# Optimization experiments

Hardware: AMD Instinct MI355X
Metric: run time of the kernel (lower is better)

The kernel has to match this reference:

```python
import jax, jax.numpy as jnp
import numpy as np

N_NODES = 50000
N_EDGES = 800000
IN_CH = 128
HID = 128
N_GRAPHS = 512


def setup_inputs() -> dict:
    key = jax.random.key(0)
    ks = jax.random.split(key, 12)
    x = jax.random.normal(ks[0], (N_NODES, IN_CH), dtype=jnp.float32)
    edge_index = jax.random.randint(ks[1], (2, N_EDGES), 0, N_NODES, dtype=jnp.int64)
    batch = jnp.sort(jax.random.randint(ks[2], (N_NODES,), 0, N_GRAPHS, dtype=jnp.int64))
    s = 0.05
    params = {
        'W1l': jax.random.normal(ks[3], (HID, IN_CH), dtype=jnp.float32) * s,
        'W1r': jax.random.normal(ks[4], (HID, IN_CH), dtype=jnp.float32) * s,
        'b1': jax.random.normal(ks[5], (HID,), dtype=jnp.float32) * s,
        'W2l': jax.random.normal(ks[6], (HID, HID), dtype=jnp.float32) * s,
        'W2r': jax.random.normal(ks[7], (HID, HID), dtype=jnp.float32) * s,
        'b2': jax.random.normal(ks[8], (HID,), dtype=jnp.float32) * s,
        'W3l': jax.random.normal(ks[9], (HID, HID), dtype=jnp.float32) * s,
        'W3r': jax.random.normal(ks[10], (HID, HID), dtype=jnp.float32) * s,
        'b3': jax.random.normal(ks[11], (HID,), dtype=jnp.float32) * s,
    }
    return {'x': x, 'edge_index': edge_index, 'batch': batch, **params}


def reference(x, edge_index, batch, W1l, W1r, b1, W2l, W2r, b2, W3l, W3r, b3):
    src = edge_index[0]
    dst = edge_index[1]
    n = x.shape[0]
    # in-degree for mean aggregation (nodes with no in-edges get 0 aggregate)
    deg = jax.ops.segment_sum(jnp.ones((src.shape[0],), x.dtype), dst, num_segments=n)
    inv_deg = (1.0 / jnp.maximum(deg, 1.0))[:, None]  # [N,1]

    def sage(h, Wl, Wr, b):
        # gather neighbor feats, scatter-mean to targets, then linear + root term
        agg = jax.ops.segment_sum(h[src], dst, num_segments=n) * inv_deg  # [N,d]
        return agg @ Wl.T + h @ Wr.T + b

    h = jax.nn.relu(sage(x, W1l, W1r, b1))
    h = jax.nn.relu(sage(h, W2l, W2r, b2))
    h = jax.nn.relu(sage(h, W3l, W3r, b3))

    # global mean pool over graph ids
    counts = jax.ops.segment_sum(jnp.ones((n,), h.dtype), batch, num_segments=N_GRAPHS)
    pooled = jax.ops.segment_sum(h, batch, num_segments=N_GRAPHS)
    return pooled / jnp.maximum(counts, 1.0)[:, None]
```

## Files before the change

### kernel.cpp

```cpp
#include <hip/hip_runtime.h>

#define N_NODES 50000
#define NP 50048
#define N_EDGES 800000
#define N_GRAPHS 512
#define F 128
#define ELLW 64

#define FILL_BLOCKS 3125
#define CASTX_BLOCKS 3128
#define CASTW_BLOCKS 48

typedef __bf16 bf16x8 __attribute__((ext_vector_type(8)));
typedef float f32x4 __attribute__((ext_vector_type(4)));
typedef unsigned short ushort_t;
typedef unsigned int uint_t;

__device__ inline ushort_t f2bf(float f) {
    uint_t u = __float_as_uint(f);
    u += 0x7FFFu + ((u >> 16) & 1u);
    return (ushort_t)(u >> 16);
}
__device__ inline float bf2f(ushort_t u) {
    return __uint_as_float(((uint_t)u) << 16);
}
__device__ inline uint_t pack2(float a, float b) {
    return (uint_t)f2bf(a) | ((uint_t)f2bf(b) << 16);
}

__global__ __launch_bounds__(256) void k_build(
    const float* __restrict__ x,
    const float* __restrict__ w0, const float* __restrict__ w1,
    const float* __restrict__ w2, const float* __restrict__ w3,
    const float* __restrict__ w4, const float* __restrict__ w5,
    const int* __restrict__ src, const int* __restrict__ dst,
    ushort_t* __restrict__ X, ushort_t* __restrict__ WB,
    int* __restrict__ cnt, ushort_t* __restrict__ ell) {
    int b = blockIdx.x;
    int t = threadIdx.x;
    if (b < FILL_BLOCKS) {
        int e = b * 256 + t;
        int d = dst[e];
        int pos = atomicAdd(&cnt[d], 1);
        if (pos < ELLW) ell[(d << 6) + pos] = (ushort_t)src[e];
    } else if (b < FILL_BLOCKS + CASTX_BLOCKS) {
        int i = ((b - FILL_BLOCKS) * 256 + t) * 8;
        uint4 o = make_uint4(0, 0, 0, 0);
        if (i < N_NODES * F) {
            float4 v0 = *(const float4*)&x[i];
            float4 v1 = *(const float4*)&x[i + 4];
            o = make_uint4(pack2(v0.x, v0.y), pack2(v0.z, v0.w),
                           pack2(v1.x, v1.y), pack2(v1.z, v1.w));
        }
        *(uint4*)&X[i] = o;
    } else {
        int idx = (b - FILL_BLOCKS - CASTX_BLOCKS) * 256 + t;
        int m = idx >> 11;
        int o = (idx & 2047) * 8;
        const float* s = w0;
        if (m == 1) s = w1; else if (m == 2) s = w2; else if (m == 3) s = w3;
        else if (m == 4) s = w4; else if (m == 5) s = w5;
        float4 v0 = *(const float4*)&s[o];
        float4 v1 = *(const float4*)&s[o + 4];
        *(uint4*)&WB[m * 16384 + o] =
            make_uint4(pack2(v0.x, v0.y), pack2(v0.z, v0.w),
                       pack2(v1.x, v1.y), pack2(v1.z, v1.w));
    }
}

__device__ inline void addrow(float* a, uint4 v) {
    a[0] += __uint_as_float(v.x << 16); a[1] += __uint_as_float(v.x & 0xFFFF0000u);
    a[2] += __uint_as_float(v.y << 16); a[3] += __uint_as_float(v.y & 0xFFFF0000u);
    a[4] += __uint_as_float(v.z << 16); a[5] += __uint_as_float(v.z & 0xFFFF0000u);
    a[6] += __uint_as_float(v.w << 16); a[7] += __uint_as_float(v.w & 0xFFFF0000u);
}

__global__ __launch_bounds__(256) void k_gather(const ushort_t* __restrict__ h,
                                                const ushort_t* __restrict__ ell,
                                                const int* __restrict__ cnt,
                                                ushort_t* __restrict__ agg) {
    int t = blockIdx.x * 256 + threadIdx.x;
    int n = t >> 4;
    int lane = t & 15;
    if (n >= N_NODES) return;
    int deg = min(cnt[n], ELLW);
    const ushort_t* el = ell + (n << 6);
    const uint4* h4 = (const uint4*)h;
    float ax[8], ay[8];
#pragma unroll
    for (int j = 0; j < 8; j++) { ax[j] = 0.f; ay[j] = 0.f; }
    int i = 0;
    for (; i + 8 <= deg; i += 8) {
        uint4 iv = *(const uint4*)&el[i];
        int s0 = iv.x & 0xFFFF, s1 = iv.x >> 16;
        int s2 = iv.y & 0xFFFF, s3 = iv.y >> 16;
        int s4 = iv.z & 0xFFFF, s5 = iv.z >> 16;
        int s6 = iv.w & 0xFFFF, s7 = iv.w >> 16;
        uint4 v0 = h4[(size_t)s0 * 16 + lane];
        uint4 v1 = h4[(size_t)s1 * 16 + lane];
        uint4 v2 = h4[(size_t)s2 * 16 + lane];
        uint4 v3 = h4[(size_t)s3 * 16 + lane];
        uint4 v4 = h4[(size_t)s4 * 16 + lane];
        uint4 v5 = h4[(size_t)s5 * 16 + lane];
        uint4 v6 = h4[(size_t)s6 * 16 + lane];
        uint4 v7 = h4[(size_t)s7 * 16 + lane];
        addrow(ax, v0); addrow(ay, v1); addrow(ax, v2); addrow(ay, v3);
        addrow(ax, v4); addrow(ay, v5); addrow(ax, v6); addrow(ay, v7);
    }
    for (; i < deg; i++) {
        uint4 v0 = h4[(size_t)el[i] * 16 + lane];
        addrow(ax, v0);
    }
    float sc = 1.0f / fmaxf((float)deg, 1.0f);
    uint_t r[4];
#pragma unroll
    for (int j = 0; j < 4; j++)
        r[j] = pack2((ax[2 * j] + ay[2 * j]) * sc,
                     (ax[2 * j + 1] + ay[2 * j + 1]) * sc);
    ((uint4*)agg)[(size_t)n * 16 + lane] = make_uint4(r[0], r[1], r[2], r[3]);
}

__global__ __launch_bounds__(256) void k_linear(const ushort_t* __restrict__ agg,
                                                const ushort_t* h,
                                                const ushort_t* __restrict__ Wl,
                                                const ushort_t* __restrict__ Wr,
                                                const float* __restrict__ bias,
                                                ushort_t* out) {
    __shared__ uint4 Alds4[512];
    __shared__ uint4 Blds4[1024];
    ushort_t* Alds = (ushort_t*)Alds4;
    ushort_t* Blds = (ushort_t*)Blds4;

    int t = threadIdx.x;
    int w = t >> 6;
    int lane = t & 63;
    int bm = blockIdx.x * 64;
    int wm = (w & 1) * 32;
    int wn = (w >> 1) * 64;
    int lrow = lane & 15;
    int kg = lane >> 4;

    f32x4 acc[2][4];
#pragma unroll
    for (int i = 0; i < 2; i++)
#pragma unroll
        for (int j = 0; j < 4; j++) acc[i][j] = (f32x4){0.f, 0.f, 0.f, 0.f};

    for (int iter = 0; iter < 4; iter++) {
        int kk = iter * 64;
        const ushort_t* A = (kk < 128) ? agg : h;
        const ushort_t* W = (kk < 128) ? Wl : Wr;
        int k0 = kk & 127;

        __syncthreads();
#pragma unroll
        for (int p = 0; p < 2; p++) {
            int chunkA = p * 4 + w;
            const ushort_t* gA = A + (size_t)(bm + lane) * F + k0 + chunkA * 8;
            ushort_t* lA = Alds + (size_t)(chunkA * 64) * 8;
            __builtin_amdgcn_global_load_lds(
                (const __attribute__((address_space(1))) void*)gA,
                (__attribute__((address_space(3))) void*)lA, 16, 0, 0);
        }
#pragma unroll
        for (int p = 0; p < 4; p++) {
            int chunkB = p * 2 + (w >> 1);
            int rbase = (w & 1) * 64;
            const ushort_t* gB = W + (size_t)(rbase + lane) * F + k0 + chunkB * 8;
            ushort_t* lB = Blds + (size_t)(chunkB * 128 + rbase) * 8;
            __builtin_amdgcn_global_load_lds(
                (const __attribute__((address_space(1))) void*)gB,
                (__attribute__((address_space(3))) void*)lB, 16, 0, 0);
        }
        __syncthreads();

#pragma unroll
        for (int ks = 0; ks < 2; ks++) {
            bf16x8 af[2], bfr[4];
#pragma unroll
            for (int i = 0; i < 2; i++)
                af[i] = *(const bf16x8*)(Alds +
                    (size_t)((ks * 4 + kg) * 64 + wm + i * 16 + lrow) * 8);
#pragma unroll
            for (int j = 0; j < 4; j++)
                bfr[j] = *(const bf16x8*)(Blds +
                    (size_t)((ks * 4 + kg) * 128 + wn + j * 16 + lrow) * 8);
#pragma unroll
            for (int i = 0; i < 2; i++)
#pragma unroll
                for (int j = 0; j < 4; j++)
                    acc[i][j] = __builtin_amdgcn_mfma_f32_16x16x32_bf16(
                        af[i], bfr[j], acc[i][j], 0, 0, 0);
        }
    }

    int quad = lane >> 4;
#pragma unroll
    for (int j = 0; j < 4; j++) {
        int c = wn + j * 16 + lrow;
        float bj = bias[c];
#pragma unroll
        for (int i = 0; i < 2; i++) {
#pragma unroll
            for (int r = 0; r < 4; r++) {
                int row = bm + wm + i * 16 + quad * 4 + r;
                if (row < N_NODES) {
                    float v = fmaxf(acc[i][j][r] + bj, 0.0f);
                    out[(size_t)row * F + c] = f2bf(v);
                }
            }
        }
    }
}

__global__ __launch_bounds__(128) void k_pool(const ushort_t* __restrict__ h,
                                              const int* __restrict__ batch,
                                              float* __restrict__ out) {
    int g = blockIdx.x;
    int j = threadIdx.x;
    int lo = 0, hi = N_NODES;
    while (lo < hi) {
        int m = (lo + hi) >> 1;
        if (batch[m] < g) lo = m + 1; else hi = m;
    }
    int start = lo;
    lo = start; hi = N_NODES;
    while (lo < hi) {
        int m = (lo + hi) >> 1;
        if (batch[m] < g + 1) lo = m + 1; else hi = m;
    }
    int end = lo;
    float s = 0.0f;
    for (int n = start; n < end; n++) s += bf2f(h[(size_t)n * F + j]);
    out[g * F + j] = s / fmaxf((float)(end - start), 1.0f);
}

extern "C" void kernel_launch(void* const* d_in, const int* in_sizes, int n_in,
                              void* d_out, int out_size, void* d_ws, size_t ws_size,
                              hipStream_t stream) {
    const float* x   = (const float*)d_in[0];
    const int*   ei  = (const int*)d_in[1];
    const int* batch = (const int*)d_in[2];
    const float* W1l = (const float*)d_in[3];
    const float* W1r = (const float*)d_in[4];
    const float* b1  = (const float*)d_in[5];
    const float* W2l = (const float*)d_in[6];
    const float* W2r = (const float*)d_in[7];
    const float* b2  = (const float*)d_in[8];
    const float* W3l = (const float*)d_in[9];
    const float* W3r = (const float*)d_in[10];
    const float* b3  = (const float*)d_in[11];
    float* out = (float*)d_out;

    const int* src = ei;
    const int* dst = ei + N_EDGES;

    ushort_t* X   = (ushort_t*)d_ws;
    ushort_t* H   = X + (size_t)NP * F;
    ushort_t* AGG = H + (size_t)NP * F;
    ushort_t* WB  = AGG + (size_t)NP * F;
    int* cnt = (int*)(WB + 6 * 16384);
    ushort_t* ell = (ushort_t*)(cnt + 50176);

    const ushort_t* Wb1l = WB;
    const ushort_t* Wb1r = WB + 16384;
    const ushort_t* Wb2l = WB + 2 * 16384;
    const ushort_t* Wb2r = WB + 3 * 16384;
    const ushort_t* Wb3l = WB + 4 * 16384;
    const ushort_t* Wb3r = WB + 5 * 16384;

    hipMemsetAsync(cnt, 0, 50176 * sizeof(int), stream);
    k_build<<<FILL_BLOCKS + CASTX_BLOCKS + CASTW_BLOCKS, 256, 0, stream>>>(
        x, W1l, W1r, W2l, W2r, W3l, W3r, src, dst, X, WB, cnt, ell);

    const int gatherBlocks = (N_NODES * 16 + 255) / 256;
    const int linearBlocks = NP / 64;

    k_gather<<<gatherBlocks, 256, 0, stream>>>(X, ell, cnt, AGG);
    k_linear<<<linearBlocks, 256, 0, stream>>>(AGG, X, Wb1l, Wb1r, b1, H);
    k_gather<<<gatherBlocks, 256, 0, stream>>>(H, ell, cnt, AGG);
    k_linear<<<linearBlocks, 256, 0, stream>>>(AGG, H, Wb2l, Wb2r, b2, H);
    k_gather<<<gatherBlocks, 256, 0, stream>>>(H, ell, cnt, AGG);
    k_linear<<<linearBlocks, 256, 0, stream>>>(AGG, H, Wb3l, Wb3r, b3, H);

    k_pool<<<N_GRAPHS, 128, 0, stream>>>(H, batch, out);
}
```

Baseline: 336.0 us.

## Widen linear K tiles, ping-pong hidden buffers, split pool rows, shorten gather unroll

The linear kernel now stages the full 128-wide K slice of each operand in LDS, using two iterations instead of four. That halves the barrier count and doubles shared memory per block. Hidden activations ping-pong between two buffers, so the linear kernel no longer reads and writes the same array in place. The pool kernel splits each graph's node rows across two thread halves and combines them through LDS. The gather inner loop drops from 8 to 4 neighbours with scalar index loads, which lowers register pressure but also reduces memory-level parallelism.

New measurement: 313.4 us. 6.7% less time.

```diff
diff --git a/kernel.cpp b/kernel.cpp
--- a/kernel.cpp
+++ b/kernel.cpp
@@ -26,6 +26,12 @@
 }
 __device__ inline uint_t pack2(float a, float b) {
     return (uint_t)f2bf(a) | ((uint_t)f2bf(b) << 16);
+}
+__device__ inline void addrow(float* a, uint4 v) {
+    a[0] += __uint_as_float(v.x << 16); a[1] += __uint_as_float(v.x & 0xFFFF0000u);
+    a[2] += __uint_as_float(v.y << 16); a[3] += __uint_as_float(v.y & 0xFFFF0000u);
+    a[4] += __uint_as_float(v.z << 16); a[5] += __uint_as_float(v.z & 0xFFFF0000u);
+    a[6] += __uint_as_float(v.w << 16); a[7] += __uint_as_float(v.w & 0xFFFF0000u);
 }
 
 __global__ __launch_bounds__(256) void k_build(
@@ -42,7 +48,7 @@
         int e = b * 256 + t;
         int d = dst[e];
         int pos = atomicAdd(&cnt[d], 1);
-        if (pos < ELLW) ell[(d << 6) + pos] = (ushort_t)src[e];
+        if (pos < ELLW) ell[((size_t)d << 6) + pos] = (ushort_t)src[e];
     } else if (b < FILL_BLOCKS + CASTX_BLOCKS) {
         int i = ((b - FILL_BLOCKS) * 256 + t) * 8;
         uint4 o = make_uint4(0, 0, 0, 0);
@@ -68,56 +74,39 @@
     }
 }
 
-__device__ inline void addrow(float* a, uint4 v) {
-    a[0] += __uint_as_float(v.x << 16); a[1] += __uint_as_float(v.x & 0xFFFF0000u);
-    a[2] += __uint_as_float(v.y << 16); a[3] += __uint_as_float(v.y & 0xFFFF0000u);
-    a[4] += __uint_as_float(v.z << 16); a[5] += __uint_as_float(v.z & 0xFFFF0000u);
-    a[6] += __uint_as_float(v.w << 16); a[7] += __uint_as_float(v.w & 0xFFFF0000u);
-}
-
 __global__ __launch_bounds__(256) void k_gather(const ushort_t* __restrict__ h,
                                                 const ushort_t* __restrict__ ell,
                                                 const int* __restrict__ cnt,
                                                 ushort_t* __restrict__ agg) {
     int t = blockIdx.x * 256 + threadIdx.x;
     int n = t >> 4;
-    int lane = t & 15;
+    int lane16 = t & 15;
     if (n >= N_NODES) return;
     int deg = min(cnt[n], ELLW);
-    const ushort_t* el = ell + (n << 6);
+    const ushort_t* el = ell + ((size_t)n << 6);
     const uint4* h4 = (const uint4*)h;
     float ax[8], ay[8];
 #pragma unroll
     for (int j = 0; j < 8; j++) { ax[j] = 0.f; ay[j] = 0.f; }
     int i = 0;
-    for (; i + 8 <= deg; i += 8) {
-        uint4 iv = *(const uint4*)&el[i];
-        int s0 = iv.x & 0xFFFF, s1 = iv.x >> 16;
-        int s2 = iv.y & 0xFFFF, s3 = iv.y >> 16;
-        int s4 = iv.z & 0xFFFF, s5 = iv.z >> 16;
-        int s6 = iv.w & 0xFFFF, s7 = iv.w >> 16;
-        uint4 v0 = h4[(size_t)s0 * 16 + lane];
-        uint4 v1 = h4[(size_t)s1 * 16 + lane];
-        uint4 v2 = h4[(size_t)s2 * 16 + lane];
-        uint4 v3 = h4[(size_t)s3 * 16 + lane];
-        uint4 v4 = h4[(size_t)s4 * 16 + lane];
-        uint4 v5 = h4[(size_t)s5 * 16 + lane];
-        uint4 v6 = h4[(size_t)s6 * 16 + lane];
-        uint4 v7 = h4[(size_t)s7 * 16 + lane];
+    for (; i + 4 <= deg; i += 4) {
+        int s0 = el[i], s1 = el[i + 1], s2 = el[i + 2], s3 = el[i + 3];
+        uint4 v0 = h4[(size_t)s0 * 16 + lane16];
+        uint4 v1 = h4[(size_t)s1 * 16 + lane16];
+        uint4 v2 = h4[(size_t)s2 * 16 + lane16];
+        uint4 v3 = h4[(size_t)s3 * 16 + lane16];
         addrow(ax, v0); addrow(ay, v1); addrow(ax, v2); addrow(ay, v3);
-        addrow(ax, v4); addrow(ay, v5); addrow(ax, v6); addrow(ay, v7);
     }
     for (; i < deg; i++) {
-        uint4 v0 = h4[(size_t)el[i] * 16 + lane];
+        uint4 v0 = h4[(size_t)el[i] * 16 + lane16];
         addrow(ax, v0);
     }
     float sc = 1.0f / fmaxf((float)deg, 1.0f);
-    uint_t r[4];
-#pragma unroll
-    for (int j = 0; j < 4; j++)
-        r[j] = pack2((ax[2 * j] + ay[2 * j]) * sc,
-                     (ax[2 * j + 1] + ay[2 * j + 1]) * sc);
-    ((uint4*)agg)[(size_t)n * 16 + lane] = make_uint4(r[0], r[1], r[2], r[3]);
+    ((uint4*)agg)[(size_t)n * 16 + lane16] = make_uint4(
+        pack2((ax[0] + ay[0]) * sc, (ax[1] + ay[1]) * sc),
+        pack2((ax[2] + ay[2]) * sc, (ax[3] + ay[3]) * sc),
+        pack2((ax[4] + ay[4]) * sc, (ax[5] + ay[5]) * sc),
+        pack2((ax[6] + ay[6]) * sc, (ax[7] + ay[7]) * sc));
 }
 
 __global__ __launch_bounds__(256) void k_linear(const ushort_t* __restrict__ agg,
@@ -126,8 +115,8 @@
                                                 const ushort_t* __restrict__ Wr,
                                                 const float* __restrict__ bias,
                                                 ushort_t* out) {
-    __shared__ uint4 Alds4[512];
-    __shared__ uint4 Blds4[1024];
+    __shared__ uint4 Alds4[1024];
+    __shared__ uint4 Blds4[2048];
     ushort_t* Alds = (ushort_t*)Alds4;
     ushort_t* Blds = (ushort_t*)Blds4;
 
@@ -146,27 +135,26 @@
 #pragma unroll
         for (int j = 0; j < 4; j++) acc[i][j] = (f32x4){0.f, 0.f, 0.f, 0.f};
 
-    for (int iter = 0; iter < 4; iter++) {
-        int kk = iter * 64;
-        const ushort_t* A = (kk < 128) ? agg : h;
-        const ushort_t* W = (kk < 128) ? Wl : Wr;
-        int k0 = kk & 127;
+#pragma unroll
+    for (int iter = 0; iter < 2; iter++) {
+        const ushort_t* A = iter ? h : agg;
+        const ushort_t* W = iter ? Wr : Wl;
 
         __syncthreads();
 #pragma unroll
-        for (int p = 0; p < 2; p++) {
+        for (int p = 0; p < 4; p++) {
             int chunkA = p * 4 + w;
-            const ushort_t* gA = A + (size_t)(bm + lane) * F + k0 + chunkA * 8;
+            const ushort_t* gA = A + (size_t)(bm + lane) * F + chunkA * 8;
             ushort_t* lA = Alds + (size_t)(chunkA * 64) * 8;
             __builtin_amdgcn_global_load_lds(
                 (const __attribute__((address_space(1))) void*)gA,
                 (__attribute__((address_space(3))) void*)lA, 16, 0, 0);
         }
 #pragma unroll
-        for (int p = 0; p < 4; p++) {
+        for (int p = 0; p < 8; p++) {
             int chunkB = p * 2 + (w >> 1);
             int rbase = (w & 1) * 64;
-            const ushort_t* gB = W + (size_t)(rbase + lane) * F + k0 + chunkB * 8;
+            const ushort_t* gB = W + (size_t)(rbase + lane) * F + chunkB * 8;
             ushort_t* lB = Blds + (size_t)(chunkB * 128 + rbase) * 8;
             __builtin_amdgcn_global_load_lds(
                 (const __attribute__((address_space(1))) void*)gB,
@@ -175,7 +163,7 @@
         __syncthreads();
 
 #pragma unroll
-        for (int ks = 0; ks < 2; ks++) {
+        for (int ks = 0; ks < 4; ks++) {
             bf16x8 af[2], bfr[4];
 #pragma unroll
             for (int i = 0; i < 2; i++)
@@ -213,11 +201,14 @@
     }
 }
 
-__global__ __launch_bounds__(128) void k_pool(const ushort_t* __restrict__ h,
+__global__ __launch_bounds__(256) void k_pool(const ushort_t* __restrict__ h,
                                               const int* __restrict__ batch,
                                               float* __restrict__ out) {
+    __shared__ float red[128];
     int g = blockIdx.x;
-    int j = threadIdx.x;
+    int t = threadIdx.x;
+    int col = t & 127;
+    int half = t >> 7;
     int lo = 0, hi = N_NODES;
     while (lo < hi) {
         int m = (lo + hi) >> 1;
@@ -231,8 +222,12 @@
     }
     int end = lo;
     float s = 0.0f;
-    for (int n = start; n < end; n++) s += bf2f(h[(size_t)n * F + j]);
-    out[g * F + j] = s / fmaxf((float)(end - start), 1.0f);
+    for (int n = start + half; n < end; n += 2)
+        s += bf2f(h[(size_t)n * F + col]);
+    if (half) red[col] = s;
+    __syncthreads();
+    if (!half)
+        out[g * F + col] = (s + red[col]) / fmaxf((float)(end - start), 1.0f);
 }
 
 extern "C" void kernel_launch(void* const* d_in, const int* in_sizes, int n_in,
@@ -256,8 +251,9 @@
     const int* dst = ei + N_EDGES;
 
     ushort_t* X   = (ushort_t*)d_ws;
-    ushort_t* H   = X + (size_t)NP * F;
-    ushort_t* AGG = H + (size_t)NP * F;
+    ushort_t* HA  = X + (size_t)NP * F;
+    ushort_t* HB  = HA + (size_t)NP * F;
+    ushort_t* AGG = HB + (size_t)NP * F;
     ushort_t* WB  = AGG + (size_t)NP * F;
     int* cnt = (int*)(WB + 6 * 16384);
     ushort_t* ell = (ushort_t*)(cnt + 50176);
@@ -277,11 +273,11 @@
     const int linearBlocks = NP / 64;
 
     k_gather<<<gatherBlocks, 256, 0, stream>>>(X, ell, cnt, AGG);
-    k_linear<<<linearBlocks, 256, 0, stream>>>(AGG, X, Wb1l, Wb1r, b1, H);
-    k_gather<<<gatherBlocks, 256, 0, stream>>>(H, ell, cnt, AGG);
-    k_linear<<<linearBlocks, 256, 0, stream>>>(AGG, H, Wb2l, Wb2r, b2, H);
-    k_gather<<<gatherBlocks, 256, 0, stream>>>(H, ell, cnt, AGG);
-    k_linear<<<linearBlocks, 256, 0, stream>>>(AGG, H, Wb3l, Wb3r, b3, H);
-
-    k_pool<<<N_GRAPHS, 128, 0, stream>>>(H, batch, out);
-}
+    k_linear<<<linearBlocks, 256, 0, stream>>>(AGG, X, Wb1l, Wb1r, b1, HA);
+    k_gather<<<gatherBlocks, 256, 0, stream>>>(HA, ell, cnt, AGG);
+    k_linear<<<linearBlocks, 256, 0, stream>>>(AGG, HA, Wb2l, Wb2r, b2, HB);
+    k_gather<<<gatherBlocks, 256, 0, stream>>>(HB, ell, cnt, AGG);
+    k_linear<<<linearBlocks, 256, 0, stream>>>(AGG, HB, Wb3l, Wb3r, b3, HA);
+
+    k_pool<<<N_GRAPHS, 256, 0, stream>>>(HA, batch, out);
+}
```
